# Kernel tuning notes

Hardware: AMD Instinct MI355X
Metric: run time of the kernel (lower is better)

Reference implementation:

```python
import jax, jax.numpy as jnp
import numpy as np

D_MODEL = 512
N_HEADS = 8
HEAD_DIM = D_MODEL // N_HEADS
MAX_LEN = 250  # relative table has 2*MAX_LEN-1 = 499 rows
B, L = 2, 2048


def setup_inputs() -> dict:
    rng = jax.random.key(0)
    ks = jax.random.split(rng, 10)
    w = 1.0 / np.sqrt(D_MODEL)
    return {
        "query": jax.random.normal(ks[0], (B, L, D_MODEL), jnp.float32),
        "key": jax.random.normal(ks[1], (B, L, D_MODEL), jnp.float32),
        "value": jax.random.normal(ks[2], (B, L, D_MODEL), jnp.float32),
        "mask": jax.random.randint(ks[3], (B, L), 0, 2, jnp.int32),
        # weights stored as [in, out]; apply as x @ W + b (equivalent to torch Linear)
        "Wq": jax.random.normal(ks[4], (D_MODEL, D_MODEL), jnp.float32) * w,
        "bq": jnp.zeros((D_MODEL,), jnp.float32),
        "Wk": jax.random.normal(ks[5], (D_MODEL, D_MODEL), jnp.float32) * w,
        "bk": jnp.zeros((D_MODEL,), jnp.float32),
        "Wv": jax.random.normal(ks[6], (D_MODEL, D_MODEL), jnp.float32) * w,
        "bv": jnp.zeros((D_MODEL,), jnp.float32),
        "Wo": jax.random.normal(ks[7], (D_MODEL, D_MODEL), jnp.float32) * w,
        "bo": jnp.zeros((D_MODEL,), jnp.float32),
        "rel_table": jax.random.normal(ks[8], (2 * MAX_LEN - 1, HEAD_DIM), jnp.float32),
    }


def reference(query, key, value, mask, Wq, bq, Wk, bk, Wv, bv, Wo, bo, rel_table):
    b, l, d = query.shape
    hd = d // N_HEADS

    def split_heads(x):  # [b,l,d] -> [b,h,l,hd]
        return x.reshape(b, l, N_HEADS, hd).transpose(0, 2, 1, 3)

    Q = split_heads(query @ Wq + bq)
    K = split_heads(key @ Wk + bk)
    V = split_heads(value @ Wv + bv)

    scores = jnp.einsum('bhid,bhjd->bhij', Q, K) / jnp.sqrt(jnp.float32(hd))

    # relative position indices: idx[i,j] = clamp(j - i + MAX_LEN-1, 0, 2*MAX_LEN-2)
    pos = jnp.arange(l)
    idx = jnp.clip(pos[None, :] - pos[:, None] + MAX_LEN - 1, 0, 2 * MAX_LEN - 2)
    rel = rel_table[idx]  # [l, l, hd] gather
    # Shaw-style additive relative-position bias (per-pair scalar from Q . rel)
    scores = scores + jnp.einsum('bhid,ijd->bhij', Q, rel)

    # key-padding mask: [b,l] -> [b,1,1,l]
    scores = jnp.where(mask[:, None, None, :] == 0, jnp.float32(-1e10), scores)

    weights = jax.nn.softmax(scores, axis=-1)  # [b,h,l,l]
    out = jnp.einsum('bhij,bhjd->bhid', weights, V)
    out = out.transpose(0, 2, 1, 3).reshape(b, l, d)
    return out @ Wo + bo
```

## Files before the change

kernel.cpp:

```cpp
#include <hip/hip_runtime.h>
#include <math.h>

#define NREL 499
#define NREL_PAD 500
#define LDB 72
#define LDT 72

typedef __attribute__((ext_vector_type(8))) short bf16x8;
typedef __attribute__((ext_vector_type(4))) float f32x4;

__device__ __forceinline__ float bf2f(ushort x) {
  union { unsigned u; float f; } v; v.u = ((unsigned)x) << 16; return v.f;
}
__device__ __forceinline__ ushort f2bf(float x) {
  union { float f; unsigned u; } v; v.f = x;
  return (ushort)((v.u + 0x8000u) >> 16);
}
__device__ __forceinline__ bf16x8 pack8(float4 a, float4 b) {
  bf16x8 r;
  r[0] = (short)f2bf(a.x); r[1] = (short)f2bf(a.y);
  r[2] = (short)f2bf(a.z); r[3] = (short)f2bf(a.w);
  r[4] = (short)f2bf(b.x); r[5] = (short)f2bf(b.y);
  r[6] = (short)f2bf(b.z); r[7] = (short)f2bf(b.w);
  return r;
}

__global__ __launch_bounds__(256) void cast_bf16(const float* __restrict__ q,
                                                 const float* __restrict__ k,
                                                 const float* __restrict__ v,
                                                 ushort* __restrict__ dst) {
  const int z = blockIdx.z;
  const float* src = (z == 0) ? q : (z == 1) ? k : v;
  const size_t base = ((size_t)blockIdx.x * 256 + threadIdx.x) * 8;
  float4 a = *(const float4*)(src + base);
  float4 b = *(const float4*)(src + base + 4);
  *(bf16x8*)(dst + (size_t)z * 2097152 + base) = pack8(a, b);
}

__global__ __launch_bounds__(256) void prep_wt(const float* __restrict__ W0,
                                               const float* __restrict__ W1,
                                               const float* __restrict__ W2,
                                               const float* __restrict__ W3,
                                               const int* __restrict__ mask,
                                               ushort* __restrict__ Wt,
                                               ushort* __restrict__ maskbf) {
  __shared__ float T[64][68];
  const int t = threadIdx.x;
  const int k0 = blockIdx.x * 64, n0 = blockIdx.y * 64, z = blockIdx.z;
  const float* W = (z == 0) ? W0 : (z == 1) ? W1 : (z == 2) ? W2 : W3;
#pragma unroll
  for (int s = 0; s < 4; ++s) {
    int idx = t + s * 256;
    int r = idx >> 4, c4 = (idx & 15) << 2;
    *(float4*)&T[r][c4] = *(const float4*)(W + (size_t)(k0 + r) * 512 + n0 + c4);
  }
  if (blockIdx.x == 0 && blockIdx.y == 0) {
    int base = z * 1024 + t * 4;
    int4 mv = *(const int4*)(mask + base);
    ushort4 mo;
    mo.x = mv.x ? 0x3F80 : 0; mo.y = mv.y ? 0x3F80 : 0;
    mo.z = mv.z ? 0x3F80 : 0; mo.w = mv.w ? 0x3F80 : 0;
    *(ushort4*)(maskbf + base) = mo;
  }
  __syncthreads();
#pragma unroll
  for (int s = 0; s < 4; ++s) {
    int idx = t + s * 256;
    int row = idx >> 4, c4 = (idx & 15) << 2;
    ushort4 u = make_ushort4(f2bf(T[c4 + 0][row]), f2bf(T[c4 + 1][row]),
                             f2bf(T[c4 + 2][row]), f2bf(T[c4 + 3][row]));
    *(ushort4*)(Wt + (size_t)z * 262144 + (size_t)(n0 + row) * 512 + k0 + c4) = u;
  }
}

template <int MODE>
__device__ __forceinline__ void gemm_tile_body(const ushort* __restrict__ A,
                                               const ushort* __restrict__ Wt,
                                               const float* __restrict__ bias,
                                               const int* __restrict__ mvec,
                                               void* __restrict__ outv,
                                               int bx, int by) {
  __shared__ ushort As[64 * LDT];
  __shared__ ushort Bs[64 * LDT];
  const int t = threadIdx.x;
  const int lane = t & 63, wave = t >> 6;
  const int m16 = lane & 15, quad = lane >> 4;
  const int koff = quad << 3;
  const int i0 = by * 64, n0 = bx * 64;
  const int row0 = t >> 3, off0 = (t & 7) << 3;
  const int row1 = (t + 256) >> 3, off1 = ((t + 256) & 7) << 3;
  const ushort* Ab = A + (size_t)i0 * 512;
  const ushort* Bb = Wt + (size_t)n0 * 512;

  uint4 ar0 = *(const uint4*)(Ab + (size_t)row0 * 512 + off0);
  uint4 ar1 = *(const uint4*)(Ab + (size_t)row1 * 512 + off1);
  uint4 br0 = *(const uint4*)(Bb + (size_t)row0 * 512 + off0);
  uint4 br1 = *(const uint4*)(Bb + (size_t)row1 * 512 + off1);

  f32x4 acc[4] = {{0.f, 0.f, 0.f, 0.f}, {0.f, 0.f, 0.f, 0.f},
                  {0.f, 0.f, 0.f, 0.f}, {0.f, 0.f, 0.f, 0.f}};

  for (int ks = 0; ks < 8; ++ks) {
    __syncthreads();
    *(uint4*)&As[row0 * LDT + off0] = ar0;
    *(uint4*)&As[row1 * LDT + off1] = ar1;
    *(uint4*)&Bs[row0 * LDT + off0] = br0;
    *(uint4*)&Bs[row1 * LDT + off1] = br1;
    __syncthreads();

    const int kn = ((ks + 1) & 7) << 6;
    uint4 an0 = *(const uint4*)(Ab + (size_t)row0 * 512 + kn + off0);
    uint4 an1 = *(const uint4*)(Ab + (size_t)row1 * 512 + kn + off1);
    uint4 bn0 = *(const uint4*)(Bb + (size_t)row0 * 512 + kn + off0);
    uint4 bn1 = *(const uint4*)(Bb + (size_t)row1 * 512 + kn + off1);

    __builtin_amdgcn_s_setprio(1);
    if (MODE != 1) {
#pragma unroll
      for (int kh = 0; kh < 2; ++kh) {
        bf16x8 af = *(const bf16x8*)&As[((wave << 4) + m16) * LDT + (kh << 5) + koff];
#pragma unroll
        for (int nt = 0; nt < 4; ++nt) {
          bf16x8 wf = *(const bf16x8*)&Bs[((nt << 4) + m16) * LDT + (kh << 5) + koff];
          acc[nt] = __builtin_amdgcn_mfma_f32_16x16x32_bf16(af, wf, acc[nt], 0, 0, 0);
        }
      }
    } else {
#pragma unroll
      for (int kh = 0; kh < 2; ++kh) {
        bf16x8 wf = *(const bf16x8*)&Bs[((wave << 4) + m16) * LDT + (kh << 5) + koff];
#pragma unroll
        for (int it = 0; it < 4; ++it) {
          bf16x8 af = *(const bf16x8*)&As[((it << 4) + m16) * LDT + (kh << 5) + koff];
          acc[it] = __builtin_amdgcn_mfma_f32_16x16x32_bf16(wf, af, acc[it], 0, 0, 0);
        }
      }
    }
    __builtin_amdgcn_s_setprio(0);

    ar0 = an0; ar1 = an1; br0 = bn0; br1 = bn1;
  }

  if (MODE == 0) {
    float* out = (float*)outv;
#pragma unroll
    for (int nt = 0; nt < 4; ++nt) {
      float bn = bias[n0 + (nt << 4) + m16];
#pragma unroll
      for (int r = 0; r < 4; ++r) {
        int i = i0 + (wave << 4) + (quad << 2) + r;
        out[(size_t)i * 512 + n0 + (nt << 4) + m16] = acc[nt][r] + bn;
      }
    }
  } else if (MODE == 2) {
    ushort* out = (ushort*)outv;
    const int b = i0 >> 11, l0 = i0 & 2047, h = n0 >> 6;
#pragma unroll
    for (int nt = 0; nt < 4; ++nt) {
      float bn = bias[n0 + (nt << 4) + m16];
      int d = (nt << 4) + m16;
#pragma unroll
      for (int r = 0; r < 4; ++r) {
        int il = (wave << 4) + (quad << 2) + r;
        out[((size_t)(b * 8 + h) * 2048 + l0 + il) * 64 + d] = f2bf(acc[nt][r] + bn);
      }
    }
  } else {
    ushort* out = (ushort*)outv;
    const int b = i0 >> 11, l0 = i0 & 2047, h = n0 >> 6;
    float4 b4 = *(const float4*)(bias + n0 + (wave << 4) + (quad << 2));
    float bb[4] = {b4.x, b4.y, b4.z, b4.w};
    float mkf[4];
#pragma unroll
    for (int it = 0; it < 4; ++it)
      mkf[it] = (mvec[b * 2048 + l0 + (it << 4) + m16] != 0) ? 1.f : 0.f;
#pragma unroll
    for (int r = 0; r < 4; ++r) {
      int d = (wave << 4) + (quad << 2) + r;
#pragma unroll
      for (int it = 0; it < 4; ++it) {
        out[((size_t)(b * 8 + h) * 64 + d) * 2048 + l0 + (it << 4) + m16] =
            f2bf((acc[it][r] + bb[r]) * mkf[it]);
      }
    }
  }
}

template <int MODE>
__global__ __launch_bounds__(256) void gemm_tile(const ushort* __restrict__ A,
                                                 const ushort* __restrict__ Wt,
                                                 const float* __restrict__ bias,
                                                 void* __restrict__ outv) {
  gemm_tile_body<MODE>(A, Wt, bias, nullptr, outv, blockIdx.x, blockIdx.y);
}

__global__ __launch_bounds__(256) void gemm_qkv(
    const ushort* __restrict__ Abf, const ushort* __restrict__ Wt,
    const float* __restrict__ bq, const float* __restrict__ bk,
    const float* __restrict__ bv, const int* __restrict__ mask,
    ushort* __restrict__ Qw, ushort* __restrict__ Kw, ushort* __restrict__ Vtw) {
  const int z = blockIdx.z;
  if (z == 0) {
    gemm_tile_body<2>(Abf, Wt, bq, nullptr, (void*)Qw, blockIdx.x, blockIdx.y);
  } else if (z == 1) {
    gemm_tile_body<2>(Abf + 2097152, Wt + 262144, bk, nullptr, (void*)Kw,
                      blockIdx.x, blockIdx.y);
  } else {
    gemm_tile_body<1>(Abf + 2 * 2097152, Wt + 2 * 262144, bv, mask, (void*)Vtw,
                      blockIdx.x, blockIdx.y);
  }
}

__global__ __launch_bounds__(256) void qrel_mfma(const ushort* __restrict__ Qw,
                                                 const float* __restrict__ rel,
                                                 float* __restrict__ qrel) {
  const int t = threadIdx.x;
  const int lane = t & 63, wave = t >> 6;
  const int m16 = lane & 15, quad = lane >> 4;
  const int r0 = blockIdx.x * 64;
  const int i0 = blockIdx.y * 64;
  const int bh = blockIdx.z;
  const ushort* Qb = Qw + ((size_t)bh * 2048 + i0 + (wave << 4) + m16) * 64;
  bf16x8 qa0 = *(const bf16x8*)(Qb + (quad << 3));
  bf16x8 qa1 = *(const bf16x8*)(Qb + 32 + (quad << 3));

  f32x4 acc[4] = {{0.f, 0.f, 0.f, 0.f}, {0.f, 0.f, 0.f, 0.f},
                  {0.f, 0.f, 0.f, 0.f}, {0.f, 0.f, 0.f, 0.f}};
#pragma unroll
  for (int rt = 0; rt < 4; ++rt) {
    int rr = min(r0 + (rt << 4) + m16, NREL - 1);
    const float* rp = rel + (size_t)rr * 64 + (quad << 3);
    bf16x8 rf0 = pack8(*(const float4*)rp, *(const float4*)(rp + 4));
    bf16x8 rf1 = pack8(*(const float4*)(rp + 32), *(const float4*)(rp + 36));
    acc[rt] = __builtin_amdgcn_mfma_f32_16x16x32_bf16(qa0, rf0, acc[rt], 0, 0, 0);
    acc[rt] = __builtin_amdgcn_mfma_f32_16x16x32_bf16(qa1, rf1, acc[rt], 0, 0, 0);
  }
#pragma unroll
  for (int rt = 0; rt < 4; ++rt) {
    int r = r0 + (rt << 4) + m16;
    if (r < NREL_PAD) {
#pragma unroll
      for (int rg = 0; rg < 4; ++rg) {
        int i = i0 + (wave << 4) + (quad << 2) + rg;
        qrel[((size_t)bh * 2048 + i) * NREL_PAD + r] = acc[rt][rg];
      }
    }
  }
}

__device__ __forceinline__ void gather_qv(float qv[4][4],
                                          const float* __restrict__ qrow,
                                          int iq, int iw0, int j0, int quad) {
  if (j0 - iw0 >= 264) {
    float e = qrow[NREL - 1];
#pragma unroll
    for (int jt = 0; jt < 4; ++jt)
#pragma unroll
      for (int r = 0; r < 4; ++r) qv[jt][r] = e;
  } else if (iw0 - j0 >= 312) {
    float e = qrow[0];
#pragma unroll
    for (int jt = 0; jt < 4; ++jt)
#pragma unroll
      for (int r = 0; r < 4; ++r) qv[jt][r] = e;
  } else {
#pragma unroll
    for (int jt = 0; jt < 4; ++jt) {
#pragma unroll
      for (int r = 0; r < 4; ++r) {
        int j = j0 + (jt << 4) + (quad << 2) + r;
        int rr = min(NREL - 1, max(0, j - iq + (NREL / 2)));
        qv[jt][r] = qrow[rr];
      }
    }
  }
}

__global__ __launch_bounds__(256) void flash_attn(
    const ushort* __restrict__ Qw, const ushort* __restrict__ Kw,
    const ushort* __restrict__ Vt, const float* __restrict__ qrel,
    const ushort* __restrict__ maskbf, ushort* __restrict__ attnbf) {
  __shared__ ushort QPs[64 * LDB];
  __shared__ ushort Ks[64 * LDB];
  __shared__ ushort Vs[64 * LDB];
  const int t = threadIdx.x;
  const int lane = t & 63, wave = t >> 6;
  const int m16 = lane & 15, quad = lane >> 4;
  const int koff = quad << 3;
  const int i0 = blockIdx.x * 64;
  const int bh = blockIdx.y;
  const int b = bh >> 3, h = bh & 7;
  const ushort* Qb = Qw + (size_t)bh * 2048 * 64;
  const ushort* Kb = Kw + (size_t)bh * 2048 * 64;
  const ushort* Vb = Vt + (size_t)bh * 64 * 2048;
  const ushort* mbf = maskbf + b * 2048;
  const int iw0 = i0 + (wave << 4);
  const int iq = iw0 + m16;
  const float* qrow = qrel + ((size_t)bh * 2048 + iq) * NREL_PAD;

  const int row0 = t >> 3, off0 = (t & 7) << 3;
  const int row1 = (t + 256) >> 3, off1 = ((t + 256) & 7) << 3;

  *(uint4*)&QPs[row0 * LDB + off0] =
      *(const uint4*)(Qb + (size_t)(i0 + row0) * 64 + off0);
  *(uint4*)&QPs[row1 * LDB + off1] =
      *(const uint4*)(Qb + (size_t)(i0 + row1) * 64 + off1);
  __syncthreads();

  bf16x8 qa0 = *(const bf16x8*)&QPs[((wave << 4) + m16) * LDB + koff];
  bf16x8 qa1 = *(const bf16x8*)&QPs[((wave << 4) + m16) * LDB + 32 + koff];

  uint4 kr0 = *(const uint4*)(Kb + (size_t)row0 * 64 + off0);
  uint4 kr1 = *(const uint4*)(Kb + (size_t)row1 * 64 + off1);
  uint4 vr0 = *(const uint4*)(Vb + (size_t)row0 * 2048 + off0);
  uint4 vr1 = *(const uint4*)(Vb + (size_t)row1 * 2048 + off1);
  bf16x8 mfr0 = *(const bf16x8*)(mbf + koff);
  bf16x8 mfr1 = *(const bf16x8*)(mbf + 32 + koff);
  float qv[4][4];
  gather_qv(qv, qrow, iq, iw0, 0, quad);

  float m_i = -INFINITY;
  f32x4 oacc[4];
  f32x4 lacc = {0.f, 0.f, 0.f, 0.f};
#pragma unroll
  for (int dt = 0; dt < 4; ++dt) oacc[dt] = (f32x4){0.f, 0.f, 0.f, 0.f};

  for (int j0 = 0; j0 < 2048; j0 += 64) {
    __syncthreads();
    *(uint4*)&Ks[row0 * LDB + off0] = kr0;
    *(uint4*)&Ks[row1 * LDB + off1] = kr1;
    *(uint4*)&Vs[row0 * LDB + off0] = vr0;
    *(uint4*)&Vs[row1 * LDB + off1] = vr1;
    __syncthreads();

    const int jn = (j0 + 64) & 2047;
    uint4 kn0 = *(const uint4*)(Kb + (size_t)(jn + row0) * 64 + off0);
    uint4 kn1 = *(const uint4*)(Kb + (size_t)(jn + row1) * 64 + off1);
    uint4 vn0 = *(const uint4*)(Vb + (size_t)row0 * 2048 + jn + off0);
    uint4 vn1 = *(const uint4*)(Vb + (size_t)row1 * 2048 + jn + off1);
    bf16x8 mfn0 = *(const bf16x8*)(mbf + jn + koff);
    bf16x8 mfn1 = *(const bf16x8*)(mbf + jn + 32 + koff);
    float qn[4][4];
    gather_qv(qn, qrow, iq, iw0, jn, quad);

    f32x4 sacc[4];
    __builtin_amdgcn_s_setprio(1);
#pragma unroll
    for (int jt = 0; jt < 4; ++jt) {
      bf16x8 kb0 = *(const bf16x8*)&Ks[((jt << 4) + m16) * LDB + koff];
      bf16x8 kb1 = *(const bf16x8*)&Ks[((jt << 4) + m16) * LDB + 32 + koff];
      f32x4 z = {0.f, 0.f, 0.f, 0.f};
      z = __builtin_amdgcn_mfma_f32_16x16x32_bf16(kb0, qa0, z, 0, 0, 0);
      z = __builtin_amdgcn_mfma_f32_16x16x32_bf16(kb1, qa1, z, 0, 0, 0);
      sacc[jt] = z;
    }
    __builtin_amdgcn_s_setprio(0);

    float sv[4][4];
#pragma unroll
    for (int jt = 0; jt < 4; ++jt)
#pragma unroll
      for (int r = 0; r < 4; ++r)
        sv[jt][r] = sacc[jt][r] * 0.125f + qv[jt][r];

    float t0 = fmaxf(fmaxf(sv[0][0], sv[0][1]), fmaxf(sv[0][2], sv[0][3]));
    float t1 = fmaxf(fmaxf(sv[1][0], sv[1][1]), fmaxf(sv[1][2], sv[1][3]));
    float t2 = fmaxf(fmaxf(sv[2][0], sv[2][1]), fmaxf(sv[2][2], sv[2][3]));
    float t3 = fmaxf(fmaxf(sv[3][0], sv[3][1]), fmaxf(sv[3][2], sv[3][3]));
    float mx = fmaxf(fmaxf(t0, t1), fmaxf(t2, t3));
    mx = fmaxf(mx, __shfl_xor(mx, 16));
    mx = fmaxf(mx, __shfl_xor(mx, 32));
    float mnew = fmaxf(m_i, mx);
    float al = __expf(m_i - mnew);
    m_i = mnew;

    const int prow = ((wave << 4) + m16) * LDB;
#pragma unroll
    for (int jt = 0; jt < 4; ++jt) {
      ushort4 pk;
      pk.x = f2bf(__expf(sv[jt][0] - mnew));
      pk.y = f2bf(__expf(sv[jt][1] - mnew));
      pk.z = f2bf(__expf(sv[jt][2] - mnew));
      pk.w = f2bf(__expf(sv[jt][3] - mnew));
      *(ushort4*)&QPs[prow + (jt << 4) + (quad << 2)] = pk;
    }

#pragma unroll
    for (int dt = 0; dt < 4; ++dt)
#pragma unroll
      for (int r = 0; r < 4; ++r) oacc[dt][r] *= al;
#pragma unroll
    for (int r = 0; r < 4; ++r) lacc[r] *= al;

    __asm__ volatile("s_waitcnt lgkmcnt(0)" ::: "memory");

    bf16x8 pa0 = *(const bf16x8*)&QPs[prow + koff];
    bf16x8 pa1 = *(const bf16x8*)&QPs[prow + 32 + koff];
    __builtin_amdgcn_s_setprio(1);
    lacc = __builtin_amdgcn_mfma_f32_16x16x32_bf16(mfr0, pa0, lacc, 0, 0, 0);
    lacc = __builtin_amdgcn_mfma_f32_16x16x32_bf16(mfr1, pa1, lacc, 0, 0, 0);
#pragma unroll
    for (int dt = 0; dt < 4; ++dt) {
      bf16x8 vb0 = *(const bf16x8*)&Vs[((dt << 4) + m16) * LDB + koff];
      bf16x8 vb1 = *(const bf16x8*)&Vs[((dt << 4) + m16) * LDB + 32 + koff];
      oacc[dt] = __builtin_amdgcn_mfma_f32_16x16x32_bf16(vb0, pa0, oacc[dt], 0, 0, 0);
      oacc[dt] = __builtin_amdgcn_mfma_f32_16x16x32_bf16(vb1, pa1, oacc[dt], 0, 0, 0);
    }
    __builtin_amdgcn_s_setprio(0);

    kr0 = kn0; kr1 = kn1; vr0 = vn0; vr1 = vn1;
    mfr0 = mfn0; mfr1 = mfn1;
#pragma unroll
    for (int jt = 0; jt < 4; ++jt)
#pragma unroll
      for (int r = 0; r < 4; ++r) qv[jt][r] = qn[jt][r];
  }

  float inv = 1.0f / lacc[0];
  ushort* dst = attnbf + (size_t)(b * 2048 + iq) * 512 + h * 64;
#pragma unroll
  for (int dt = 0; dt < 4; ++dt) {
    ushort4 st;
    st.x = f2bf(oacc[dt][0] * inv);
    st.y = f2bf(oacc[dt][1] * inv);
    st.z = f2bf(oacc[dt][2] * inv);
    st.w = f2bf(oacc[dt][3] * inv);
    *(ushort4*)(dst + (dt << 4) + (quad << 2)) = st;
  }
}

extern "C" void kernel_launch(void* const* d_in, const int* in_sizes, int n_in,
                              void* d_out, int out_size, void* d_ws,
                              size_t ws_size, hipStream_t stream) {
  const float* query = (const float*)d_in[0];
  const float* key   = (const float*)d_in[1];
  const float* value = (const float*)d_in[2];
  const int*   mask  = (const int*)d_in[3];
  const float* Wq = (const float*)d_in[4];
  const float* bq = (const float*)d_in[5];
  const float* Wk = (const float*)d_in[6];
  const float* bk = (const float*)d_in[7];
  const float* Wv = (const float*)d_in[8];
  const float* bv = (const float*)d_in[9];
  const float* Wo = (const float*)d_in[10];
  const float* bo = (const float*)d_in[11];
  const float* rel = (const float*)d_in[12];

  char* w = (char*)d_ws;
  size_t off = 0;
  ushort* Qw  = (ushort*)(w + off); off += (size_t)16 * 2048 * 64 * 2;
  ushort* Kw  = (ushort*)(w + off); off += (size_t)16 * 2048 * 64 * 2;
  ushort* Vtw = (ushort*)(w + off); off += (size_t)16 * 64 * 2048 * 2;
  ushort* Wt  = (ushort*)(w + off); off += (size_t)4 * 512 * 512 * 2;
  float* qrel = (float*)(w + off);  off += (size_t)16 * 2048 * NREL_PAD * 4;
  ushort* attnbf = (ushort*)(w + off); off += (size_t)4096 * 512 * 2;
  ushort* Abf = (ushort*)(w + off); off += (size_t)3 * 4096 * 512 * 2;
  ushort* maskbf = (ushort*)(w + off); off += (size_t)2 * 2048 * 2;
  float* out = (float*)d_out;

  dim3 bb(256);
  hipLaunchKernelGGL(cast_bf16, dim3(1024, 1, 3), bb, 0, stream, query, key,
                     value, Abf);
  hipLaunchKernelGGL(prep_wt, dim3(8, 8, 4), bb, 0, stream, Wq, Wk, Wv, Wo,
                     mask, Wt, maskbf);
  hipLaunchKernelGGL(gemm_qkv, dim3(8, 64, 3), bb, 0, stream, Abf, Wt, bq, bk,
                     bv, mask, Qw, Kw, Vtw);
  hipLaunchKernelGGL(qrel_mfma, dim3(8, 32, 16), bb, 0, stream, Qw, rel, qrel);
  hipLaunchKernelGGL(flash_attn, dim3(32, 16), bb, 0, stream, Qw, Kw, Vtw, qrel,
                     maskbf, attnbf);
  hipLaunchKernelGGL((gemm_tile<0>), dim3(8, 64), bb, 0, stream, attnbf,
                     Wt + 3 * 262144, bo, (void*)out);
}
```

Baseline: 232.8 us.

## Widen attention KV tile to 128, fold scales, lazy softmax rescale, swizzle blocks

Result: slower. 285.4 us (+22.6%).

```diff
diff --git a/kernel.cpp b/kernel.cpp
--- a/kernel.cpp
+++ b/kernel.cpp
@@ -3,8 +3,11 @@
 
 #define NREL 499
 #define NREL_PAD 500
-#define LDB 72
 #define LDT 72
+#define KVB 128
+#define LDK 72
+#define LDV 136
+#define LDP 136
 
 typedef __attribute__((ext_vector_type(8))) short bf16x8;
 typedef __attribute__((ext_vector_type(4))) float f32x4;
@@ -79,7 +82,7 @@
                                                const float* __restrict__ bias,
                                                const int* __restrict__ mvec,
                                                void* __restrict__ outv,
-                                               int bx, int by) {
+                                               int bx, int by, float oscale) {
   __shared__ ushort As[64 * LDT];
   __shared__ ushort Bs[64 * LDT];
   const int t = threadIdx.x;
@@ -162,7 +165,8 @@
 #pragma unroll
       for (int r = 0; r < 4; ++r) {
         int il = (wave << 4) + (quad << 2) + r;
-        out[((size_t)(b * 8 + h) * 2048 + l0 + il) * 64 + d] = f2bf(acc[nt][r] + bn);
+        out[((size_t)(b * 8 + h) * 2048 + l0 + il) * 64 + d] =
+            f2bf((acc[nt][r] + bn) * oscale);
       }
     }
   } else {
@@ -191,7 +195,7 @@
                                                  const ushort* __restrict__ Wt,
                                                  const float* __restrict__ bias,
                                                  void* __restrict__ outv) {
-  gemm_tile_body<MODE>(A, Wt, bias, nullptr, outv, blockIdx.x, blockIdx.y);
+  gemm_tile_body<MODE>(A, Wt, bias, nullptr, outv, blockIdx.x, blockIdx.y, 1.f);
 }
 
 __global__ __launch_bounds__(256) void gemm_qkv(
@@ -201,13 +205,14 @@
     ushort* __restrict__ Qw, ushort* __restrict__ Kw, ushort* __restrict__ Vtw) {
   const int z = blockIdx.z;
   if (z == 0) {
-    gemm_tile_body<2>(Abf, Wt, bq, nullptr, (void*)Qw, blockIdx.x, blockIdx.y);
+    gemm_tile_body<2>(Abf, Wt, bq, nullptr, (void*)Qw, blockIdx.x, blockIdx.y,
+                      0.125f);
   } else if (z == 1) {
     gemm_tile_body<2>(Abf + 2097152, Wt + 262144, bk, nullptr, (void*)Kw,
-                      blockIdx.x, blockIdx.y);
+                      blockIdx.x, blockIdx.y, 1.f);
   } else {
     gemm_tile_body<1>(Abf + 2 * 2097152, Wt + 2 * 262144, bv, mask, (void*)Vtw,
-                      blockIdx.x, blockIdx.y);
+                      blockIdx.x, blockIdx.y, 1.f);
   }
 }
 
@@ -230,8 +235,14 @@
   for (int rt = 0; rt < 4; ++rt) {
     int rr = min(r0 + (rt << 4) + m16, NREL - 1);
     const float* rp = rel + (size_t)rr * 64 + (quad << 3);
-    bf16x8 rf0 = pack8(*(const float4*)rp, *(const float4*)(rp + 4));
-    bf16x8 rf1 = pack8(*(const float4*)(rp + 32), *(const float4*)(rp + 36));
+    float4 a0 = *(const float4*)rp,        a1 = *(const float4*)(rp + 4);
+    float4 a2 = *(const float4*)(rp + 32), a3 = *(const float4*)(rp + 36);
+    a0.x *= 8.f; a0.y *= 8.f; a0.z *= 8.f; a0.w *= 8.f;
+    a1.x *= 8.f; a1.y *= 8.f; a1.z *= 8.f; a1.w *= 8.f;
+    a2.x *= 8.f; a2.y *= 8.f; a2.z *= 8.f; a2.w *= 8.f;
+    a3.x *= 8.f; a3.y *= 8.f; a3.z *= 8.f; a3.w *= 8.f;
+    bf16x8 rf0 = pack8(a0, a1);
+    bf16x8 rf1 = pack8(a2, a3);
     acc[rt] = __builtin_amdgcn_mfma_f32_16x16x32_bf16(qa0, rf0, acc[rt], 0, 0, 0);
     acc[rt] = __builtin_amdgcn_mfma_f32_16x16x32_bf16(qa1, rf1, acc[rt], 0, 0, 0);
   }
@@ -248,28 +259,28 @@
   }
 }
 
-__device__ __forceinline__ void gather_qv(float qv[4][4],
+__device__ __forceinline__ void gather_qv(float qv[8][4],
                                           const float* __restrict__ qrow,
                                           int iq, int iw0, int j0, int quad) {
   if (j0 - iw0 >= 264) {
     float e = qrow[NREL - 1];
 #pragma unroll
-    for (int jt = 0; jt < 4; ++jt)
+    for (int jt = 0; jt < 8; ++jt)
 #pragma unroll
       for (int r = 0; r < 4; ++r) qv[jt][r] = e;
-  } else if (iw0 - j0 >= 312) {
+  } else if (iw0 - j0 >= 376) {
     float e = qrow[0];
 #pragma unroll
-    for (int jt = 0; jt < 4; ++jt)
+    for (int jt = 0; jt < 8; ++jt)
 #pragma unroll
       for (int r = 0; r < 4; ++r) qv[jt][r] = e;
   } else {
 #pragma unroll
-    for (int jt = 0; jt < 4; ++jt) {
+    for (int jt = 0; jt < 8; ++jt) {
 #pragma unroll
       for (int r = 0; r < 4; ++r) {
         int j = j0 + (jt << 4) + (quad << 2) + r;
-        int rr = min(NREL - 1, max(0, j - iq + (NREL / 2)));
+        int rr = min(NREL - 1, max(0, j - iq + 249));
         qv[jt][r] = qrow[rr];
       }
     }
@@ -280,15 +291,17 @@
     const ushort* __restrict__ Qw, const ushort* __restrict__ Kw,
     const ushort* __restrict__ Vt, const float* __restrict__ qrel,
     const ushort* __restrict__ maskbf, ushort* __restrict__ attnbf) {
-  __shared__ ushort QPs[64 * LDB];
-  __shared__ ushort Ks[64 * LDB];
-  __shared__ ushort Vs[64 * LDB];
+  __shared__ ushort QPs[64 * LDP];
+  __shared__ ushort Ks[KVB * LDK];
+  __shared__ ushort Vs[64 * LDV];
   const int t = threadIdx.x;
   const int lane = t & 63, wave = t >> 6;
   const int m16 = lane & 15, quad = lane >> 4;
   const int koff = quad << 3;
-  const int i0 = blockIdx.x * 64;
-  const int bh = blockIdx.y;
+  const int bid = (blockIdx.y << 5) + blockIdx.x;
+  const int swz = ((bid & 7) << 6) + (bid >> 3);
+  const int i0 = (swz & 31) << 6;
+  const int bh = swz >> 5;
   const int b = bh >> 3, h = bh & 7;
   const ushort* Qb = Qw + (size_t)bh * 2048 * 64;
   const ushort* Kb = Kw + (size_t)bh * 2048 * 64;
@@ -298,25 +311,25 @@
   const int iq = iw0 + m16;
   const float* qrow = qrel + ((size_t)bh * 2048 + iq) * NREL_PAD;
 
-  const int row0 = t >> 3, off0 = (t & 7) << 3;
-  const int row1 = (t + 256) >> 3, off1 = ((t + 256) & 7) << 3;
-
-  *(uint4*)&QPs[row0 * LDB + off0] =
-      *(const uint4*)(Qb + (size_t)(i0 + row0) * 64 + off0);
-  *(uint4*)&QPs[row1 * LDB + off1] =
-      *(const uint4*)(Qb + (size_t)(i0 + row1) * 64 + off1);
+  const int krow = t >> 3, kcol = (t & 7) << 3;
+  const int vrow = t >> 4, vcol = (t & 15) << 3;
+
+  *(uint4*)&QPs[krow * LDP + kcol] =
+      *(const uint4*)(Qb + (size_t)(i0 + krow) * 64 + kcol);
+  *(uint4*)&QPs[(krow + 32) * LDP + kcol] =
+      *(const uint4*)(Qb + (size_t)(i0 + krow + 32) * 64 + kcol);
   __syncthreads();
 
-  bf16x8 qa0 = *(const bf16x8*)&QPs[((wave << 4) + m16) * LDB + koff];
-  bf16x8 qa1 = *(const bf16x8*)&QPs[((wave << 4) + m16) * LDB + 32 + koff];
-
-  uint4 kr0 = *(const uint4*)(Kb + (size_t)row0 * 64 + off0);
-  uint4 kr1 = *(const uint4*)(Kb + (size_t)row1 * 64 + off1);
-  uint4 vr0 = *(const uint4*)(Vb + (size_t)row0 * 2048 + off0);
-  uint4 vr1 = *(const uint4*)(Vb + (size_t)row1 * 2048 + off1);
-  bf16x8 mfr0 = *(const bf16x8*)(mbf + koff);
-  bf16x8 mfr1 = *(const bf16x8*)(mbf + 32 + koff);
-  float qv[4][4];
+  bf16x8 qa0 = *(const bf16x8*)&QPs[((wave << 4) + m16) * LDP + koff];
+  bf16x8 qa1 = *(const bf16x8*)&QPs[((wave << 4) + m16) * LDP + 32 + koff];
+
+  uint4 kr[4], vr[4];
+#pragma unroll
+  for (int s = 0; s < 4; ++s) {
+    kr[s] = *(const uint4*)(Kb + (size_t)(krow + s * 32) * 64 + kcol);
+    vr[s] = *(const uint4*)(Vb + (size_t)(vrow + s * 16) * 2048 + vcol);
+  }
+  float qv[8][4];
   gather_qv(qv, qrow, iq, iw0, 0, quad);
 
   float m_i = -INFINITY;
@@ -325,93 +338,98 @@
 #pragma unroll
   for (int dt = 0; dt < 4; ++dt) oacc[dt] = (f32x4){0.f, 0.f, 0.f, 0.f};
 
-  for (int j0 = 0; j0 < 2048; j0 += 64) {
+  for (int j0 = 0; j0 < 2048; j0 += KVB) {
     __syncthreads();
-    *(uint4*)&Ks[row0 * LDB + off0] = kr0;
-    *(uint4*)&Ks[row1 * LDB + off1] = kr1;
-    *(uint4*)&Vs[row0 * LDB + off0] = vr0;
-    *(uint4*)&Vs[row1 * LDB + off1] = vr1;
+#pragma unroll
+    for (int s = 0; s < 4; ++s) {
+      *(uint4*)&Ks[(krow + s * 32) * LDK + kcol] = kr[s];
+      *(uint4*)&Vs[(vrow + s * 16) * LDV + vcol] = vr[s];
+    }
     __syncthreads();
 
-    const int jn = (j0 + 64) & 2047;
-    uint4 kn0 = *(const uint4*)(Kb + (size_t)(jn + row0) * 64 + off0);
-    uint4 kn1 = *(const uint4*)(Kb + (size_t)(jn + row1) * 64 + off1);
-    uint4 vn0 = *(const uint4*)(Vb + (size_t)row0 * 2048 + jn + off0);
-    uint4 vn1 = *(const uint4*)(Vb + (size_t)row1 * 2048 + jn + off1);
-    bf16x8 mfn0 = *(const bf16x8*)(mbf + jn + koff);
-    bf16x8 mfn1 = *(const bf16x8*)(mbf + jn + 32 + koff);
-    float qn[4][4];
+    const int jn = (j0 + KVB) & 2047;
+    uint4 kn[4], vn[4];
+#pragma unroll
+    for (int s = 0; s < 4; ++s) {
+      kn[s] = *(const uint4*)(Kb + (size_t)(jn + krow + s * 32) * 64 + kcol);
+      vn[s] = *(const uint4*)(Vb + (size_t)(vrow + s * 16) * 2048 + jn + vcol);
+    }
+    bf16x8 mf[4];
+#pragma unroll
+    for (int ks = 0; ks < 4; ++ks)
+      mf[ks] = *(const bf16x8*)(mbf + j0 + (ks << 5) + koff);
+    float qn[8][4];
     gather_qv(qn, qrow, iq, iw0, jn, quad);
 
-    f32x4 sacc[4];
+    f32x4 sacc[8];
     __builtin_amdgcn_s_setprio(1);
 #pragma unroll
-    for (int jt = 0; jt < 4; ++jt) {
-      bf16x8 kb0 = *(const bf16x8*)&Ks[((jt << 4) + m16) * LDB + koff];
-      bf16x8 kb1 = *(const bf16x8*)&Ks[((jt << 4) + m16) * LDB + 32 + koff];
-      f32x4 z = {0.f, 0.f, 0.f, 0.f};
+    for (int jt = 0; jt < 8; ++jt) {
+      bf16x8 kb0 = *(const bf16x8*)&Ks[((jt << 4) + m16) * LDK + koff];
+      bf16x8 kb1 = *(const bf16x8*)&Ks[((jt << 4) + m16) * LDK + 32 + koff];
+      f32x4 z = {qv[jt][0], qv[jt][1], qv[jt][2], qv[jt][3]};
       z = __builtin_amdgcn_mfma_f32_16x16x32_bf16(kb0, qa0, z, 0, 0, 0);
       z = __builtin_amdgcn_mfma_f32_16x16x32_bf16(kb1, qa1, z, 0, 0, 0);
       sacc[jt] = z;
     }
     __builtin_amdgcn_s_setprio(0);
 
-    float sv[4][4];
-#pragma unroll
-    for (int jt = 0; jt < 4; ++jt)
-#pragma unroll
-      for (int r = 0; r < 4; ++r)
-        sv[jt][r] = sacc[jt][r] * 0.125f + qv[jt][r];
-
-    float t0 = fmaxf(fmaxf(sv[0][0], sv[0][1]), fmaxf(sv[0][2], sv[0][3]));
-    float t1 = fmaxf(fmaxf(sv[1][0], sv[1][1]), fmaxf(sv[1][2], sv[1][3]));
-    float t2 = fmaxf(fmaxf(sv[2][0], sv[2][1]), fmaxf(sv[2][2], sv[2][3]));
-    float t3 = fmaxf(fmaxf(sv[3][0], sv[3][1]), fmaxf(sv[3][2], sv[3][3]));
-    float mx = fmaxf(fmaxf(t0, t1), fmaxf(t2, t3));
+    float mj[8];
+#pragma unroll
+    for (int jt = 0; jt < 8; ++jt)
+      mj[jt] = fmaxf(fmaxf(sacc[jt][0], sacc[jt][1]),
+                     fmaxf(sacc[jt][2], sacc[jt][3]));
+    float mx = fmaxf(fmaxf(fmaxf(mj[0], mj[1]), fmaxf(mj[2], mj[3])),
+                     fmaxf(fmaxf(mj[4], mj[5]), fmaxf(mj[6], mj[7])));
     mx = fmaxf(mx, __shfl_xor(mx, 16));
     mx = fmaxf(mx, __shfl_xor(mx, 32));
-    float mnew = fmaxf(m_i, mx);
-    float al = __expf(m_i - mnew);
-    m_i = mnew;
-
-    const int prow = ((wave << 4) + m16) * LDB;
-#pragma unroll
-    for (int jt = 0; jt < 4; ++jt) {
+
+    if (__any(mx > m_i + 8.f)) {
+      float mnew = fmaxf(m_i, mx);
+      float al = __expf(m_i - mnew);
+      m_i = mnew;
+#pragma unroll
+      for (int dt = 0; dt < 4; ++dt)
+#pragma unroll
+        for (int r = 0; r < 4; ++r) oacc[dt][r] *= al;
+#pragma unroll
+      for (int r = 0; r < 4; ++r) lacc[r] *= al;
+    }
+
+    const int prow = ((wave << 4) + m16) * LDP;
+#pragma unroll
+    for (int jt = 0; jt < 8; ++jt) {
       ushort4 pk;
-      pk.x = f2bf(__expf(sv[jt][0] - mnew));
-      pk.y = f2bf(__expf(sv[jt][1] - mnew));
-      pk.z = f2bf(__expf(sv[jt][2] - mnew));
-      pk.w = f2bf(__expf(sv[jt][3] - mnew));
+      pk.x = f2bf(__expf(sacc[jt][0] - m_i));
+      pk.y = f2bf(__expf(sacc[jt][1] - m_i));
+      pk.z = f2bf(__expf(sacc[jt][2] - m_i));
+      pk.w = f2bf(__expf(sacc[jt][3] - m_i));
       *(ushort4*)&QPs[prow + (jt << 4) + (quad << 2)] = pk;
     }
-
-#pragma unroll
-    for (int dt = 0; dt < 4; ++dt)
-#pragma unroll
-      for (int r = 0; r < 4; ++r) oacc[dt][r] *= al;
-#pragma unroll
-    for (int r = 0; r < 4; ++r) lacc[r] *= al;
-
     __asm__ volatile("s_waitcnt lgkmcnt(0)" ::: "memory");
 
-    bf16x8 pa0 = *(const bf16x8*)&QPs[prow + koff];
-    bf16x8 pa1 = *(const bf16x8*)&QPs[prow + 32 + koff];
+    bf16x8 pa[4];
+#pragma unroll
+    for (int ks = 0; ks < 4; ++ks)
+      pa[ks] = *(const bf16x8*)&QPs[prow + (ks << 5) + koff];
     __builtin_amdgcn_s_setprio(1);
-    lacc = __builtin_amdgcn_mfma_f32_16x16x32_bf16(mfr0, pa0, lacc, 0, 0, 0);
-    lacc = __builtin_amdgcn_mfma_f32_16x16x32_bf16(mfr1, pa1, lacc, 0, 0, 0);
+#pragma unroll
+    for (int ks = 0; ks < 4; ++ks)
+      lacc = __builtin_amdgcn_mfma_f32_16x16x32_bf16(mf[ks], pa[ks], lacc, 0, 0, 0);
 #pragma unroll
     for (int dt = 0; dt < 4; ++dt) {
-      bf16x8 vb0 = *(const bf16x8*)&Vs[((dt << 4) + m16) * LDB + koff];
-      bf16x8 vb1 = *(const bf16x8*)&Vs[((dt << 4) + m16) * LDB + 32 + koff];
-      oacc[dt] = __builtin_amdgcn_mfma_f32_16x16x32_bf16(vb0, pa0, oacc[dt], 0, 0, 0);
-      oacc[dt] = __builtin_amdgcn_mfma_f32_16x16x32_bf16(vb1, pa1, oacc[dt], 0, 0, 0);
+#pragma unroll
+      for (int ks = 0; ks < 4; ++ks) {
+        bf16x8 vb = *(const bf16x8*)&Vs[((dt << 4) + m16) * LDV + (ks << 5) + koff];
+        oacc[dt] = __builtin_amdgcn_mfma_f32_16x16x32_bf16(vb, pa[ks], oacc[dt], 0, 0, 0);
+      }
     }
     __builtin_amdgcn_s_setprio(0);
 
-    kr0 = kn0; kr1 = kn1; vr0 = vn0; vr1 = vn1;
-    mfr0 = mfn0; mfr1 = mfn1;
-#pragma unroll
-    for (int jt = 0; jt < 4; ++jt)
+#pragma unroll
+    for (int s = 0; s < 4; ++s) { kr[s] = kn[s]; vr[s] = vn[s]; }
+#pragma unroll
+    for (int jt = 0; jt < 8; ++jt)
 #pragma unroll
       for (int r = 0; r < 4; ++r) qv[jt][r] = qn[jt][r];
   }
```

## Fold softmax scale into Q projection, seed MFMA with bias, lazy rescale

Applied to the files above, without the earlier changes.

After: 232.1 us. About the same (-0.3%).

```diff
diff --git a/kernel.cpp b/kernel.cpp
--- a/kernel.cpp
+++ b/kernel.cpp
@@ -79,7 +79,7 @@
                                                const float* __restrict__ bias,
                                                const int* __restrict__ mvec,
                                                void* __restrict__ outv,
-                                               int bx, int by) {
+                                               int bx, int by, float oscale) {
   __shared__ ushort As[64 * LDT];
   __shared__ ushort Bs[64 * LDT];
   const int t = threadIdx.x;
@@ -162,7 +162,8 @@
 #pragma unroll
       for (int r = 0; r < 4; ++r) {
         int il = (wave << 4) + (quad << 2) + r;
-        out[((size_t)(b * 8 + h) * 2048 + l0 + il) * 64 + d] = f2bf(acc[nt][r] + bn);
+        out[((size_t)(b * 8 + h) * 2048 + l0 + il) * 64 + d] =
+            f2bf((acc[nt][r] + bn) * oscale);
       }
     }
   } else {
@@ -191,7 +192,7 @@
                                                  const ushort* __restrict__ Wt,
                                                  const float* __restrict__ bias,
                                                  void* __restrict__ outv) {
-  gemm_tile_body<MODE>(A, Wt, bias, nullptr, outv, blockIdx.x, blockIdx.y);
+  gemm_tile_body<MODE>(A, Wt, bias, nullptr, outv, blockIdx.x, blockIdx.y, 1.f);
 }
 
 __global__ __launch_bounds__(256) void gemm_qkv(
@@ -201,13 +202,14 @@
     ushort* __restrict__ Qw, ushort* __restrict__ Kw, ushort* __restrict__ Vtw) {
   const int z = blockIdx.z;
   if (z == 0) {
-    gemm_tile_body<2>(Abf, Wt, bq, nullptr, (void*)Qw, blockIdx.x, blockIdx.y);
+    gemm_tile_body<2>(Abf, Wt, bq, nullptr, (void*)Qw, blockIdx.x, blockIdx.y,
+                      0.125f);
   } else if (z == 1) {
     gemm_tile_body<2>(Abf + 2097152, Wt + 262144, bk, nullptr, (void*)Kw,
-                      blockIdx.x, blockIdx.y);
+                      blockIdx.x, blockIdx.y, 1.f);
   } else {
     gemm_tile_body<1>(Abf + 2 * 2097152, Wt + 2 * 262144, bv, mask, (void*)Vtw,
-                      blockIdx.x, blockIdx.y);
+                      blockIdx.x, blockIdx.y, 1.f);
   }
 }
 
@@ -230,8 +232,14 @@
   for (int rt = 0; rt < 4; ++rt) {
     int rr = min(r0 + (rt << 4) + m16, NREL - 1);
     const float* rp = rel + (size_t)rr * 64 + (quad << 3);
-    bf16x8 rf0 = pack8(*(const float4*)rp, *(const float4*)(rp + 4));
-    bf16x8 rf1 = pack8(*(const float4*)(rp + 32), *(const float4*)(rp + 36));
+    float4 a0 = *(const float4*)rp,        a1 = *(const float4*)(rp + 4);
+    float4 a2 = *(const float4*)(rp + 32), a3 = *(const float4*)(rp + 36);
+    a0.x *= 8.f; a0.y *= 8.f; a0.z *= 8.f; a0.w *= 8.f;
+    a1.x *= 8.f; a1.y *= 8.f; a1.z *= 8.f; a1.w *= 8.f;
+    a2.x *= 8.f; a2.y *= 8.f; a2.z *= 8.f; a2.w *= 8.f;
+    a3.x *= 8.f; a3.y *= 8.f; a3.z *= 8.f; a3.w *= 8.f;
+    bf16x8 rf0 = pack8(a0, a1);
+    bf16x8 rf1 = pack8(a2, a3);
     acc[rt] = __builtin_amdgcn_mfma_f32_16x16x32_bf16(qa0, rf0, acc[rt], 0, 0, 0);
     acc[rt] = __builtin_amdgcn_mfma_f32_16x16x32_bf16(qa1, rf1, acc[rt], 0, 0, 0);
   }
@@ -269,7 +277,7 @@
 #pragma unroll
       for (int r = 0; r < 4; ++r) {
         int j = j0 + (jt << 4) + (quad << 2) + r;
-        int rr = min(NREL - 1, max(0, j - iq + (NREL / 2)));
+        int rr = min(NREL - 1, max(0, j - iq + 249));
         qv[jt][r] = qrow[rr];
       }
     }
@@ -287,8 +295,10 @@
   const int lane = t & 63, wave = t >> 6;
   const int m16 = lane & 15, quad = lane >> 4;
   const int koff = quad << 3;
-  const int i0 = blockIdx.x * 64;
-  const int bh = blockIdx.y;
+  const int bid = ((int)blockIdx.y << 5) + (int)blockIdx.x;
+  const int swz = ((bid & 7) << 6) + (bid >> 3);
+  const int i0 = (swz & 31) << 6;
+  const int bh = swz >> 5;
   const int b = bh >> 3, h = bh & 7;
   const ushort* Qb = Qw + (size_t)bh * 2048 * 64;
   const ushort* Kb = Kw + (size_t)bh * 2048 * 64;
@@ -349,49 +359,43 @@
     for (int jt = 0; jt < 4; ++jt) {
       bf16x8 kb0 = *(const bf16x8*)&Ks[((jt << 4) + m16) * LDB + koff];
       bf16x8 kb1 = *(const bf16x8*)&Ks[((jt << 4) + m16) * LDB + 32 + koff];
-      f32x4 z = {0.f, 0.f, 0.f, 0.f};
+      f32x4 z = {qv[jt][0], qv[jt][1], qv[jt][2], qv[jt][3]};
       z = __builtin_amdgcn_mfma_f32_16x16x32_bf16(kb0, qa0, z, 0, 0, 0);
       z = __builtin_amdgcn_mfma_f32_16x16x32_bf16(kb1, qa1, z, 0, 0, 0);
       sacc[jt] = z;
     }
     __builtin_amdgcn_s_setprio(0);
 
-    float sv[4][4];
-#pragma unroll
-    for (int jt = 0; jt < 4; ++jt)
-#pragma unroll
-      for (int r = 0; r < 4; ++r)
-        sv[jt][r] = sacc[jt][r] * 0.125f + qv[jt][r];
-
-    float t0 = fmaxf(fmaxf(sv[0][0], sv[0][1]), fmaxf(sv[0][2], sv[0][3]));
-    float t1 = fmaxf(fmaxf(sv[1][0], sv[1][1]), fmaxf(sv[1][2], sv[1][3]));
-    float t2 = fmaxf(fmaxf(sv[2][0], sv[2][1]), fmaxf(sv[2][2], sv[2][3]));
-    float t3 = fmaxf(fmaxf(sv[3][0], sv[3][1]), fmaxf(sv[3][2], sv[3][3]));
+    float t0 = fmaxf(fmaxf(sacc[0][0], sacc[0][1]), fmaxf(sacc[0][2], sacc[0][3]));
+    float t1 = fmaxf(fmaxf(sacc[1][0], sacc[1][1]), fmaxf(sacc[1][2], sacc[1][3]));
+    float t2 = fmaxf(fmaxf(sacc[2][0], sacc[2][1]), fmaxf(sacc[2][2], sacc[2][3]));
+    float t3 = fmaxf(fmaxf(sacc[3][0], sacc[3][1]), fmaxf(sacc[3][2], sacc[3][3]));
     float mx = fmaxf(fmaxf(t0, t1), fmaxf(t2, t3));
     mx = fmaxf(mx, __shfl_xor(mx, 16));
     mx = fmaxf(mx, __shfl_xor(mx, 32));
-    float mnew = fmaxf(m_i, mx);
-    float al = __expf(m_i - mnew);
-    m_i = mnew;
+
+    if (__any(mx > m_i + 8.f)) {
+      float mnew = fmaxf(m_i, mx);
+      float al = __expf(m_i - mnew);
+      m_i = mnew;
+#pragma unroll
+      for (int dt = 0; dt < 4; ++dt)
+#pragma unroll
+        for (int r = 0; r < 4; ++r) oacc[dt][r] *= al;
+#pragma unroll
+      for (int r = 0; r < 4; ++r) lacc[r] *= al;
+    }
 
     const int prow = ((wave << 4) + m16) * LDB;
 #pragma unroll
     for (int jt = 0; jt < 4; ++jt) {
       ushort4 pk;
-      pk.x = f2bf(__expf(sv[jt][0] - mnew));
-      pk.y = f2bf(__expf(sv[jt][1] - mnew));
-      pk.z = f2bf(__expf(sv[jt][2] - mnew));
-      pk.w = f2bf(__expf(sv[jt][3] - mnew));
+      pk.x = f2bf(__expf(sacc[jt][0] - m_i));
+      pk.y = f2bf(__expf(sacc[jt][1] - m_i));
+      pk.z = f2bf(__expf(sacc[jt][2] - m_i));
+      pk.w = f2bf(__expf(sacc[jt][3] - m_i));
       *(ushort4*)&QPs[prow + (jt << 4) + (quad << 2)] = pk;
     }
-
-#pragma unroll
-    for (int dt = 0; dt < 4; ++dt)
-#pragma unroll
-      for (int r = 0; r < 4; ++r) oacc[dt][r] *= al;
-#pragma unroll
-    for (int r = 0; r < 4; ++r) lacc[r] *= al;
-
     __asm__ volatile("s_waitcnt lgkmcnt(0)" ::: "memory");
 
     bf16x8 pa0 = *(const bf16x8*)&QPs[prow + koff];
```
